# Optimization experiments

Hardware: AMD Instinct MI355X
Metric: run time of the kernel (lower is better)

## Reference

```python
import jax, jax.numpy as jnp
import numpy as np

B, P, F, H, C, D = 512, 32, 16, 4, 32, 128   # graphs, nodes/graph, node feat, heads, head_dim, hidden
N = B * P
E_DIM = 5

def _lin(k, o, i):
    return jax.random.normal(k, (o, i)) * (1.0 / np.sqrt(i))

def setup_inputs():
    key = jax.random.key(0)
    ks = jax.random.split(key, 32)
    # fully-connected directed edges (no self loops) within each graph
    a = np.repeat(np.arange(P), P); b = np.tile(np.arange(P), P)
    m = a != b; a, b = a[m], b[m]
    off = (np.arange(B) * P)[:, None]
    src = (a[None, :] + off).reshape(-1); dst = (b[None, :] + off).reshape(-1)
    edge_index = jnp.asarray(np.stack([src, dst]), dtype=jnp.int32)
    E = src.size
    x = jax.random.normal(ks[0], (N, F))
    edge_attr = jax.random.normal(ks[1], (E, E_DIM))
    z = jnp.zeros
    return dict(
        x=x, edge_index=edge_index, edge_attr=edge_attr,
        W1l=_lin(ks[2], D, F), b1l=z(D), W1r=_lin(ks[3], D, F), b1r=z(D),
        W1e=_lin(ks[4], D, E_DIM), att1=jax.random.normal(ks[5], (1, H, C)) * 0.1, bias1=z(D),
        W2l=_lin(ks[6], D, D), b2l=z(D), W2r=_lin(ks[7], D, D), b2r=z(D),
        W2e=_lin(ks[8], D, E_DIM), att2=jax.random.normal(ks[9], (1, H, C)) * 0.1, bias2=z(D),
        Wc1=_lin(ks[10], D, D), bc1=z(D), Wc2=_lin(ks[11], 1, D), bc2=z(1),
        Ws1=_lin(ks[12], D, D), bs1=z(D), Ws2=_lin(ks[13], 1, D), bs2=z(1),
        Wn1=_lin(ks[14], D, D), bn1=z(D), Wn2=_lin(ks[15], 1, D), bn2=z(1),
    )

def _gatv2(x, src, dst, edge_attr, Wl, bl, Wr, br, We, att, bias):
    # PyG GATv2Conv, concat=True, heads=H, out_channels=C, edge_dim=E_DIM, add_self_loops=False
    E = src.shape[0]
    xl = x @ Wl.T + bl                                   # [N, H*C] messages (source side)
    xr = x @ Wr.T + br                                   # [N, H*C] destination side
    e = (xl[src] + xr[dst] + edge_attr @ We.T).reshape(E, H, C)
    g = jax.nn.leaky_relu(e, 0.2)
    score = jnp.sum(g * att, axis=-1)                    # [E, H]
    smax = jax.ops.segment_max(score, dst, num_segments=N)
    ex = jnp.exp(score - smax[dst])
    denom = jax.ops.segment_sum(ex, dst, num_segments=N)
    alpha = ex / (denom[dst] + 1e-16)                    # segment softmax over in-edges of dst
    msg = xl[src].reshape(E, H, C) * alpha[..., None]
    return jax.ops.segment_sum(msg, dst, num_segments=N).reshape(N, H * C) + bias

def _mlp(h, W1, b1, W2, b2):
    return jax.nn.relu(h @ W1.T + b1) @ W2.T + b2

def reference(x, edge_index, edge_attr, W1l, b1l, W1r, b1r, W1e, att1, bias1,
              W2l, b2l, W2r, b2r, W2e, att2, bias2,
              Wc1, bc1, Wc2, bc2, Ws1, bs1, Ws2, bs2, Wn1, bn1, Wn2, bn2):
    src, dst = edge_index[0], edge_index[1]
    h = _gatv2(x, src, dst, edge_attr, W1l, b1l, W1r, b1r, W1e, att1, bias1)
    hb = h.reshape(B, P, D)
    h = (hb - hb.mean(axis=1, keepdims=True)).reshape(N, D)   # MeanSubtractionNorm per graph
    h = jax.nn.relu(h)
    h = jax.nn.relu(_gatv2(h, src, dst, edge_attr, W2l, b2l, W2r, b2r, W2e, att2, bias2))
    g = h.reshape(B, P, D).mean(axis=1)                       # global_mean_pool (equal-size graphs)
    value = _mlp(g, Wc1, bc1, Wc2, bc2)                       # critic        [B, 1]
    src_logits = _mlp(h, Ws1, bs1, Ws2, bs2).reshape(B, P)    # source_actor, dense per graph
    noop = _mlp(g, Wn1, bn1, Wn2, bn2)                        # noop_actor    [B, 1]
    return jnp.concatenate([value, noop, src_logits], axis=1) # [B, P+2]
```

## Files before the change

kernel.cpp:

```cpp
#include <hip/hip_runtime.h>

#define PP    32
#define FF    16
#define HH    4
#define CC    32
#define DD    128
#define EDIM  5
#define EPG   992
#define NB    512

template <int CTRL>
__device__ __forceinline__ float dpp_add(float v) {
    int t = __builtin_amdgcn_update_dpp(0, __builtin_bit_cast(int, v), CTRL, 0xF, 0xF, true);
    return v + __builtin_bit_cast(float, t);
}
template <int CTRL>
__device__ __forceinline__ float dpp_mov(float v) {
    int t = __builtin_amdgcn_update_dpp(0, __builtin_bit_cast(int, v), CTRL, 0xF, 0xF, true);
    return __builtin_bit_cast(float, t);
}
__device__ __forceinline__ float red64(float v) {
    v = dpp_add<0x111>(v);
    v = dpp_add<0x112>(v);
    v = dpp_add<0x114>(v);
    v = dpp_add<0x118>(v);
    v = dpp_add<0x142>(v);
    v = dpp_add<0x143>(v);
    return v;
}
__device__ __forceinline__ float redquad(float v) {
    v = dpp_add<0xB1>(v);
    v = dpp_add<0x4E>(v);
    return v;
}
__device__ __forceinline__ float maxquad(float v) {
    v = fmaxf(v, dpp_mov<0xB1>(v));
    v = fmaxf(v, dpp_mov<0x4E>(v));
    return v;
}

__device__ __forceinline__ void attention(const float* __restrict__ eattr,
                                          const float* __restrict__ We, const float* __restrict__ att,
                                          const float* __restrict__ bias,
                                          const float* __restrict__ sMsg, const float* __restrict__ sDst,
                                          float* __restrict__ sS, float* __restrict__ sOut,
                                          int tid, long eBase, bool relu)
{
    float* __restrict__ sE = sOut;
    {
        const int s  = tid >> 4;
        const int ch0 = (tid & 15) * 8;
        float we[40], at[8], xl[8];
#pragma unroll
        for (int q = 0; q < 10; ++q)
            *(float4*)(we + q * 4) = *(const float4*)(We + ch0 * EDIM + q * 4);
        *(float4*)(at)     = *(const float4*)(att + ch0);
        *(float4*)(at + 4) = *(const float4*)(att + ch0 + 4);
        *(float4*)(xl)     = *(const float4*)(sMsg + s * DD + ch0);
        *(float4*)(xl + 4) = *(const float4*)(sMsg + s * DD + ch0 + 4);

        for (int halfd = 0; halfd < 2; ++halfd) {
            const int d0 = halfd * 16;
            {
                const int dl = tid & 15;
                const int d = d0 + dl;
                int jj = d - (d > s);
                if (jj > 30) jj = 30;
                const float* ea = eattr + (eBase + s * 31 + jj) * EDIM;
                const float e0 = ea[0], e1 = ea[1], e2 = ea[2], e3 = ea[3], e4 = ea[4];
                float* p = sE + (((s << 4) | dl) << 3);
                *(float4*)p = make_float4(e0, e1, e2, e3);
                p[4] = e4;
            }
            __syncthreads();
#pragma unroll 2
            for (int dl = 0; dl < 16; ++dl) {
                const int d = d0 + dl;
                const float* ep = sE + (((s << 4) | dl) << 3);
                const float4 ef = *(const float4*)ep;
                const float e4v = ep[4];
                float xr[8];
                *(float4*)(xr)     = *(const float4*)(sDst + d * DD + ch0);
                *(float4*)(xr + 4) = *(const float4*)(sDst + d * DD + ch0 + 4);
                float acc0 = 0.f, acc1 = 0.f;
#pragma unroll
                for (int c = 0; c < 8; ++c) {
                    float v = xl[c] + xr[c];
                    const float* w = we + c * EDIM;
                    v = fmaf(w[0], ef.x, v); v = fmaf(w[1], ef.y, v); v = fmaf(w[2], ef.z, v);
                    v = fmaf(w[3], ef.w, v); v = fmaf(w[4], e4v, v);
                    v = fmaf(0.4f, fabsf(v), 0.6f * v);
                    if (c & 1) acc1 = fmaf(v, at[c], acc1);
                    else       acc0 = fmaf(v, at[c], acc0);
                }
                const float r = redquad(acc0 + acc1);
                if ((tid & 3) == 0)
                    sS[s * DD + d * HH + ((tid >> 2) & 3)] = r;
            }
            __syncthreads();
        }
    }
    {
        const int col = tid >> 2;
        const int r   = tid & 3;
        const int dd  = col >> 2;
        float v[8];
        float mx = -3.4e38f;
#pragma unroll
        for (int i = 0; i < 8; ++i) {
            const int s = r * 8 + i;
            v[i] = sS[s * DD + col];
            mx = (s == dd) ? mx : fmaxf(mx, v[i]);
        }
        mx = maxquad(mx);
        float sum = 0.f;
#pragma unroll
        for (int i = 0; i < 8; ++i) {
            const int s = r * 8 + i;
            float ex = __expf(v[i] - mx);
            ex = (s == dd) ? 0.f : ex;
            v[i] = ex; sum += ex;
        }
        sum = redquad(sum);
        const float inv = 1.f / (sum + 1e-16f);
#pragma unroll
        for (int i = 0; i < 8; ++i)
            sS[(r * 8 + i) * DD + col] = v[i] * inv;
    }
    __syncthreads();
    {
        const int d = tid >> 4, sub = tid & 15;
#pragma unroll
        for (int half = 0; half < 2; ++half) {
            const int ch4 = half * 16 + sub;
            const int idx = d * HH + (ch4 >> 3);
            const float* bp = bias + ch4 * 4;
            float4 acc = make_float4(bp[0], bp[1], bp[2], bp[3]);
#pragma unroll
            for (int s = 0; s < PP; ++s) {
                const float a = sS[s * DD + idx];
                const float4 xv = *(const float4*)(sMsg + s * DD + ch4 * 4);
                acc.x = fmaf(a, xv.x, acc.x);
                acc.y = fmaf(a, xv.y, acc.y);
                acc.z = fmaf(a, xv.z, acc.z);
                acc.w = fmaf(a, xv.w, acc.w);
            }
            if (relu) {
                acc.x = fmaxf(acc.x, 0.f); acc.y = fmaxf(acc.y, 0.f);
                acc.z = fmaxf(acc.z, 0.f); acc.w = fmaxf(acc.w, 0.f);
            }
            *(float4*)(sOut + d * DD + ch4 * 4) = acc;
        }
    }
}

extern "C" __global__ void __launch_bounds__(512)
__attribute__((amdgpu_waves_per_eu(4, 4)))
planetwars_gnn_kernel(const float* __restrict__ x, const float* __restrict__ eattr,
                      const float* __restrict__ W1l, const float* __restrict__ b1l,
                      const float* __restrict__ W1r, const float* __restrict__ b1r,
                      const float* __restrict__ W1e, const float* __restrict__ att1, const float* __restrict__ bias1,
                      const float* __restrict__ W2l, const float* __restrict__ b2l,
                      const float* __restrict__ W2r, const float* __restrict__ b2r,
                      const float* __restrict__ W2e, const float* __restrict__ att2, const float* __restrict__ bias2,
                      const float* __restrict__ Wc1, const float* __restrict__ bc1,
                      const float* __restrict__ Wc2, const float* __restrict__ bc2,
                      const float* __restrict__ Ws1, const float* __restrict__ bs1,
                      const float* __restrict__ Ws2, const float* __restrict__ bs2,
                      const float* __restrict__ Wn1, const float* __restrict__ bn1,
                      const float* __restrict__ Wn2, const float* __restrict__ bn2,
                      float* __restrict__ out)
{
    __shared__ __align__(16) float sA[PP * DD];
    __shared__ __align__(16) float sB[PP * DD];
    __shared__ __align__(16) float sH[PP * DD];
    __shared__ __align__(16) float sU[PP * DD];

    const int tid = threadIdx.x;
    const int g = blockIdx.x;
    const long eBase = (long)g * EPG;

    sU[tid] = x[g * PP * FF + tid];
    __syncthreads();

    {
        const int j = tid & 127, d0 = (tid >> 7) * 8;
        float wl[16], wr[16];
#pragma unroll
        for (int q = 0; q < 4; ++q) {
            *(float4*)(wl + q * 4) = *(const float4*)(W1l + j * FF + q * 4);
            *(float4*)(wr + q * 4) = *(const float4*)(W1r + j * FF + q * 4);
        }
        const float bl = b1l[j], br = b1r[j];
#pragma unroll
        for (int i = 0; i < 8; ++i) {
            const float* xr = sU + (d0 + i) * FF;
            float al = bl, ar = br;
#pragma unroll
            for (int k = 0; k < FF; ++k) {
                const float xv = xr[k];
                al = fmaf(wl[k], xv, al);
                ar = fmaf(wr[k], xv, ar);
            }
            sA[(d0 + i) * DD + j] = al;
            sB[(d0 + i) * DD + j] = ar;
        }
    }
    __syncthreads();

    attention(eattr, W1e, att1, bias1, sA, sB, sU, sH, tid, eBase, false);
    __syncthreads();

    {
        const int col = tid >> 2, r = tid & 3;
        float v[8];
        float ssum = 0.f;
#pragma unroll
        for (int i = 0; i < 8; ++i) {
            v[i] = sH[(r * 8 + i) * DD + col];
            ssum += v[i];
        }
        ssum = redquad(ssum);
        const float mn = ssum * (1.0f / 32.0f);
#pragma unroll
        for (int i = 0; i < 8; ++i)
            sH[(r * 8 + i) * DD + col] = fmaxf(v[i] - mn, 0.f);
    }
    __syncthreads();

    {
        const int jj = tid & 63, d0 = (tid >> 6) * 4;
        float accL0[4], accL1[4], accR0[4], accR1[4];
        const float bl0 = b2l[jj], bl1 = b2l[jj + 64];
        const float br0 = b2r[jj], br1 = b2r[jj + 64];
#pragma unroll
        for (int i = 0; i < 4; ++i) { accL0[i] = bl0; accL1[i] = bl1; accR0[i] = br0; accR1[i] = br1; }
        const float* WL0 = W2l + jj * DD;
        const float* WL1 = W2l + (jj + 64) * DD;
        const float* WR0 = W2r + jj * DD;
        const float* WR1 = W2r + (jj + 64) * DD;
        for (int k8 = 0; k8 < 16; ++k8) {
            const float4 l00 = *(const float4*)(WL0 + k8 * 8), l01 = *(const float4*)(WL0 + k8 * 8 + 4);
            const float4 l10 = *(const float4*)(WL1 + k8 * 8), l11 = *(const float4*)(WL1 + k8 * 8 + 4);
            const float4 r00 = *(const float4*)(WR0 + k8 * 8), r01 = *(const float4*)(WR0 + k8 * 8 + 4);
            const float4 r10 = *(const float4*)(WR1 + k8 * 8), r11 = *(const float4*)(WR1 + k8 * 8 + 4);
#pragma unroll
            for (int i = 0; i < 4; ++i) {
                const float4 a0 = *(const float4*)(sH + (d0 + i) * DD + k8 * 8);
                const float4 a1 = *(const float4*)(sH + (d0 + i) * DD + k8 * 8 + 4);
                accL0[i] = fmaf(l00.x, a0.x, accL0[i]); accL0[i] = fmaf(l00.y, a0.y, accL0[i]);
                accL0[i] = fmaf(l00.z, a0.z, accL0[i]); accL0[i] = fmaf(l00.w, a0.w, accL0[i]);
                accL0[i] = fmaf(l01.x, a1.x, accL0[i]); accL0[i] = fmaf(l01.y, a1.y, accL0[i]);
                accL0[i] = fmaf(l01.z, a1.z, accL0[i]); accL0[i] = fmaf(l01.w, a1.w, accL0[i]);
                accL1[i] = fmaf(l10.x, a0.x, accL1[i]); accL1[i] = fmaf(l10.y, a0.y, accL1[i]);
                accL1[i] = fmaf(l10.z, a0.z, accL1[i]); accL1[i] = fmaf(l10.w, a0.w, accL1[i]);
                accL1[i] = fmaf(l11.x, a1.x, accL1[i]); accL1[i] = fmaf(l11.y, a1.y, accL1[i]);
                accL1[i] = fmaf(l11.z, a1.z, accL1[i]); accL1[i] = fmaf(l11.w, a1.w, accL1[i]);
                accR0[i] = fmaf(r00.x, a0.x, accR0[i]); accR0[i] = fmaf(r00.y, a0.y, accR0[i]);
                accR0[i] = fmaf(r00.z, a0.z, accR0[i]); accR0[i] = fmaf(r00.w, a0.w, accR0[i]);
                accR0[i] = fmaf(r01.x, a1.x, accR0[i]); accR0[i] = fmaf(r01.y, a1.y, accR0[i]);
                accR0[i] = fmaf(r01.z, a1.z, accR0[i]); accR0[i] = fmaf(r01.w, a1.w, accR0[i]);
                accR1[i] = fmaf(r10.x, a0.x, accR1[i]); accR1[i] = fmaf(r10.y, a0.y, accR1[i]);
                accR1[i] = fmaf(r10.z, a0.z, accR1[i]); accR1[i] = fmaf(r10.w, a0.w, accR1[i]);
                accR1[i] = fmaf(r11.x, a1.x, accR1[i]); accR1[i] = fmaf(r11.y, a1.y, accR1[i]);
                accR1[i] = fmaf(r11.z, a1.z, accR1[i]); accR1[i] = fmaf(r11.w, a1.w, accR1[i]);
            }
        }
#pragma unroll
        for (int i = 0; i < 4; ++i) {
            sA[(d0 + i) * DD + jj]      = accL0[i];
            sA[(d0 + i) * DD + jj + 64] = accL1[i];
            sB[(d0 + i) * DD + jj]      = accR0[i];
            sB[(d0 + i) * DD + jj + 64] = accR1[i];
        }
    }
    __syncthreads();

    attention(eattr, W2e, att2, bias2, sA, sB, sU, sH, tid, eBase, true);
    __syncthreads();

    {
        const int col = tid >> 2, r = tid & 3;
        float ssum = 0.f;
#pragma unroll
        for (int i = 0; i < 8; ++i) ssum += sH[(r * 8 + i) * DD + col];
        ssum = redquad(ssum);
        if (r == 0) sU[col] = ssum * (1.0f / 32.0f);
    }
    __syncthreads();

    {
        const int jj = tid & 63, d0 = (tid >> 6) * 4;
        const float b0 = bs1[jj], b1 = bs1[jj + 64];
        float acc0[4], acc1[4];
#pragma unroll
        for (int i = 0; i < 4; ++i) { acc0[i] = b0; acc1[i] = b1; }
        const float* W0 = Ws1 + jj * DD;
        const float* W1 = Ws1 + (jj + 64) * DD;
        for (int k8 = 0; k8 < 16; ++k8) {
            const float4 w00 = *(const float4*)(W0 + k8 * 8), w01 = *(const float4*)(W0 + k8 * 8 + 4);
            const float4 w10 = *(const float4*)(W1 + k8 * 8), w11 = *(const float4*)(W1 + k8 * 8 + 4);
#pragma unroll
            for (int i = 0; i < 4; ++i) {
                const float4 a0 = *(const float4*)(sH + (d0 + i) * DD + k8 * 8);
                const float4 a1 = *(const float4*)(sH + (d0 + i) * DD + k8 * 8 + 4);
                acc0[i] = fmaf(w00.x, a0.x, acc0[i]); acc0[i] = fmaf(w00.y, a0.y, acc0[i]);
                acc0[i] = fmaf(w00.z, a0.z, acc0[i]); acc0[i] = fmaf(w00.w, a0.w, acc0[i]);
                acc0[i] = fmaf(w01.x, a1.x, acc0[i]); acc0[i] = fmaf(w01.y, a1.y, acc0[i]);
                acc0[i] = fmaf(w01.z, a1.z, acc0[i]); acc0[i] = fmaf(w01.w, a1.w, acc0[i]);
                acc1[i] = fmaf(w10.x, a0.x, acc1[i]); acc1[i] = fmaf(w10.y, a0.y, acc1[i]);
                acc1[i] = fmaf(w10.z, a0.z, acc1[i]); acc1[i] = fmaf(w10.w, a0.w, acc1[i]);
                acc1[i] = fmaf(w11.x, a1.x, acc1[i]); acc1[i] = fmaf(w11.y, a1.y, acc1[i]);
                acc1[i] = fmaf(w11.z, a1.z, acc1[i]); acc1[i] = fmaf(w11.w, a1.w, acc1[i]);
            }
        }
        const float ws2a = Ws2[jj], ws2b = Ws2[jj + 64];
        const float bias2s = bs2[0];
#pragma unroll
        for (int i = 0; i < 4; ++i) {
            const float t = fmaf(fmaxf(acc0[i], 0.f), ws2a, fmaxf(acc1[i], 0.f) * ws2b);
            const float r = red64(t);
            if ((tid & 63) == 63) out[g * 34 + 2 + d0 + i] = r + bias2s;
        }
    }

    if (tid < 128) {
        const int w = tid >> 6, j = tid & 63;
        const float* Wa = (w ? Wn1 : Wc1);
        const float* ba = (w ? bn1 : bc1);
        const float* Wb = (w ? Wn2 : Wc2);
        const float  bb = (w ? bn2 : bc2)[0];
        float h0 = ba[j], h1 = ba[j + 64];
        const float* R0 = Wa + j * DD;
        const float* R1 = Wa + (j + 64) * DD;
#pragma unroll
        for (int k8 = 0; k8 < 16; ++k8) {
            const float4 g0 = *(const float4*)(sU + k8 * 8);
            const float4 g1 = *(const float4*)(sU + k8 * 8 + 4);
            const float4 p00 = *(const float4*)(R0 + k8 * 8), p01 = *(const float4*)(R0 + k8 * 8 + 4);
            const float4 p10 = *(const float4*)(R1 + k8 * 8), p11 = *(const float4*)(R1 + k8 * 8 + 4);
            h0 = fmaf(p00.x, g0.x, h0); h0 = fmaf(p00.y, g0.y, h0);
            h0 = fmaf(p00.z, g0.z, h0); h0 = fmaf(p00.w, g0.w, h0);
            h0 = fmaf(p01.x, g1.x, h0); h0 = fmaf(p01.y, g1.y, h0);
            h0 = fmaf(p01.z, g1.z, h0); h0 = fmaf(p01.w, g1.w, h0);
            h1 = fmaf(p10.x, g0.x, h1); h1 = fmaf(p10.y, g0.y, h1);
            h1 = fmaf(p10.z, g0.z, h1); h1 = fmaf(p10.w, g0.w, h1);
            h1 = fmaf(p11.x, g1.x, h1); h1 = fmaf(p11.y, g1.y, h1);
            h1 = fmaf(p11.z, g1.z, h1); h1 = fmaf(p11.w, g1.w, h1);
        }
        const float t = fmaf(fmaxf(h0, 0.f), Wb[j], fmaxf(h1, 0.f) * Wb[j + 64]);
        const float r = red64(t);
        if (j == 63) out[g * 34 + w] = r + bb;
    }
}

extern "C" void kernel_launch(void* const* d_in, const int* in_sizes, int n_in,
                              void* d_out, int out_size, void* d_ws, size_t ws_size,
                              hipStream_t stream)
{
    (void)in_sizes; (void)n_in; (void)d_ws; (void)ws_size; (void)out_size;
    planetwars_gnn_kernel<<<dim3(NB), dim3(512), 0, stream>>>(
        (const float*)d_in[0], (const float*)d_in[2],
        (const float*)d_in[3], (const float*)d_in[4], (const float*)d_in[5], (const float*)d_in[6],
        (const float*)d_in[7], (const float*)d_in[8], (const float*)d_in[9],
        (const float*)d_in[10], (const float*)d_in[11], (const float*)d_in[12], (const float*)d_in[13],
        (const float*)d_in[14], (const float*)d_in[15], (const float*)d_in[16],
        (const float*)d_in[17], (const float*)d_in[18], (const float*)d_in[19], (const float*)d_in[20],
        (const float*)d_in[21], (const float*)d_in[22], (const float*)d_in[23], (const float*)d_in[24],
        (const float*)d_in[25], (const float*)d_in[26], (const float*)d_in[27], (const float*)d_in[28],
        (float*)d_out);
}
```

Baseline: 244.7 us.

## Split fused GNN kernel into multi-kernel pipeline via workspace buffers

Replaces the single per-graph fused kernel with ten smaller launches (transforms, score, softmax, aggregation, norm, heads) that exchange intermediates through global workspace buffers. The score stage is split across two blocks per graph to raise parallelism and relieve per-block LDS/register pressure. The monolithic kernel is kept as a fallback when no workspace is provided. This adds global memory round trips and several launch overheads in exchange for more blocks and simpler kernels.

```diff
diff --git a/kernel.cpp b/kernel.cpp
--- a/kernel.cpp
+++ b/kernel.cpp
@@ -8,6 +8,9 @@
 #define EDIM  5
 #define EPG   992
 #define NB    512
+#define NN    (NB * PP)
+#define WS_SLOT 2097152
+#define WS_NEED ((size_t)4 * WS_SLOT * 4)
 
 template <int CTRL>
 __device__ __forceinline__ float dpp_add(float v) {
@@ -20,12 +23,8 @@
     return __builtin_bit_cast(float, t);
 }
 __device__ __forceinline__ float red64(float v) {
-    v = dpp_add<0x111>(v);
-    v = dpp_add<0x112>(v);
-    v = dpp_add<0x114>(v);
-    v = dpp_add<0x118>(v);
-    v = dpp_add<0x142>(v);
-    v = dpp_add<0x143>(v);
+    v = dpp_add<0x111>(v); v = dpp_add<0x112>(v); v = dpp_add<0x114>(v);
+    v = dpp_add<0x118>(v); v = dpp_add<0x142>(v); v = dpp_add<0x143>(v);
     return v;
 }
 __device__ __forceinline__ float redquad(float v) {
@@ -39,7 +38,306 @@
     return v;
 }
 
-__device__ __forceinline__ void attention(const float* __restrict__ eattr,
+
+extern "C" __global__ void __launch_bounds__(256)
+k_t1(const float* __restrict__ x,
+     const float* __restrict__ W1l, const float* __restrict__ b1l,
+     const float* __restrict__ W1r, const float* __restrict__ b1r,
+     float* __restrict__ xl, float* __restrict__ xr)
+{
+    const int idx = blockIdx.x * 256 + threadIdx.x;
+    const int n = idx >> 7, j = idx & 127;
+    float wl[16], wr[16], xv[16];
+#pragma unroll
+    for (int q = 0; q < 4; ++q) {
+        *(float4*)(wl + q * 4) = *(const float4*)(W1l + j * FF + q * 4);
+        *(float4*)(wr + q * 4) = *(const float4*)(W1r + j * FF + q * 4);
+        *(float4*)(xv + q * 4) = *(const float4*)(x + n * FF + q * 4);
+    }
+    float al = b1l[j], ar = b1r[j];
+#pragma unroll
+    for (int k = 0; k < FF; ++k) {
+        al = fmaf(wl[k], xv[k], al);
+        ar = fmaf(wr[k], xv[k], ar);
+    }
+    xl[idx] = al;
+    xr[idx] = ar;
+}
+
+extern "C" __global__ void __launch_bounds__(512)
+k_score(const float* __restrict__ xl, const float* __restrict__ xr,
+        const float* __restrict__ eattr,
+        const float* __restrict__ We, const float* __restrict__ att,
+        float* __restrict__ sc)
+{
+    const int b = blockIdx.x;
+    const int g = b >> 1, halfd = b & 1;
+    const int tid = threadIdx.x;
+    const int s   = tid >> 4;
+    const int h   = (tid >> 2) & 3;
+    const int ch0 = (tid & 15) * 8;
+    const long eBase = (long)g * EPG;
+
+    float we[40], at[8], xlv[8];
+#pragma unroll
+    for (int q = 0; q < 10; ++q)
+        *(float4*)(we + q * 4) = *(const float4*)(We + ch0 * EDIM + q * 4);
+    *(float4*)(at)      = *(const float4*)(att + ch0);
+    *(float4*)(at + 4)  = *(const float4*)(att + ch0 + 4);
+    *(float4*)(xlv)     = *(const float4*)(xl + (g * PP + s) * DD + ch0);
+    *(float4*)(xlv + 4) = *(const float4*)(xl + (g * PP + s) * DD + ch0 + 4);
+
+    const int d0 = halfd * 16;
+    for (int dl = 0; dl < 16; ++dl) {
+        const int d = d0 + dl;
+        int jj = d - (d > s);
+        if (jj > 30) jj = 30;
+        const float* ea = eattr + (eBase + s * 31 + jj) * EDIM;
+        const float e0 = ea[0], e1 = ea[1], e2 = ea[2], e3 = ea[3], e4 = ea[4];
+        float xrv[8];
+        *(float4*)(xrv)     = *(const float4*)(xr + (g * PP + d) * DD + ch0);
+        *(float4*)(xrv + 4) = *(const float4*)(xr + (g * PP + d) * DD + ch0 + 4);
+        float acc0 = 0.f, acc1 = 0.f;
+#pragma unroll
+        for (int c = 0; c < 8; ++c) {
+            float v = xlv[c] + xrv[c];
+            const float* w = we + c * EDIM;
+            v = fmaf(w[0], e0, v); v = fmaf(w[1], e1, v); v = fmaf(w[2], e2, v);
+            v = fmaf(w[3], e3, v); v = fmaf(w[4], e4, v);
+            v = fmaf(0.4f, fabsf(v), 0.6f * v);
+            if (c & 1) acc1 = fmaf(v, at[c], acc1);
+            else       acc0 = fmaf(v, at[c], acc0);
+        }
+        const float r = redquad(acc0 + acc1);
+        if ((tid & 3) == 0)
+            sc[(((long)(g * PP + d) << 2) + h) * PP + s] = r;
+    }
+}
+
+extern "C" __global__ void __launch_bounds__(256)
+k_softmax(float* __restrict__ sc)
+{
+    const int idx = blockIdx.x * 256 + threadIdx.x;
+    const int col = idx >> 2;
+    const int r   = idx & 3;
+    const int dd  = (col >> 2) & 31;
+    float* base = sc + (long)col * PP;
+    float v[8];
+    float mx = -3.4e38f;
+#pragma unroll
+    for (int i = 0; i < 8; ++i) {
+        const int s = r * 8 + i;
+        v[i] = base[s];
+        mx = (s == dd) ? mx : fmaxf(mx, v[i]);
+    }
+    mx = maxquad(mx);
+    float sum = 0.f;
+#pragma unroll
+    for (int i = 0; i < 8; ++i) {
+        const int s = r * 8 + i;
+        float ex = __expf(v[i] - mx);
+        ex = (s == dd) ? 0.f : ex;
+        v[i] = ex; sum += ex;
+    }
+    sum = redquad(sum);
+    const float inv = 1.f / (sum + 1e-16f);
+#pragma unroll
+    for (int i = 0; i < 8; ++i)
+        base[r * 8 + i] = v[i] * inv;
+}
+
+extern "C" __global__ void __launch_bounds__(256)
+k_agg(const float* __restrict__ alpha, const float* __restrict__ msg,
+      const float* __restrict__ bias, float* __restrict__ hout, const int relu)
+{
+    const int idx = blockIdx.x * 256 + threadIdx.x;
+    const int n = idx >> 5, ch4 = idx & 31;
+    const int g = n >> 5;
+    const int h = ch4 >> 3;
+    const float* ap = alpha + (((long)n << 2) + h) * PP;
+    const float* bp = bias + ch4 * 4;
+    float4 acc = make_float4(bp[0], bp[1], bp[2], bp[3]);
+#pragma unroll
+    for (int s = 0; s < PP; ++s) {
+        const float a = ap[s];
+        const float4 xv = *(const float4*)(msg + (g * PP + s) * DD + ch4 * 4);
+        acc.x = fmaf(a, xv.x, acc.x);
+        acc.y = fmaf(a, xv.y, acc.y);
+        acc.z = fmaf(a, xv.z, acc.z);
+        acc.w = fmaf(a, xv.w, acc.w);
+    }
+    if (relu) {
+        acc.x = fmaxf(acc.x, 0.f); acc.y = fmaxf(acc.y, 0.f);
+        acc.z = fmaxf(acc.z, 0.f); acc.w = fmaxf(acc.w, 0.f);
+    }
+    *(float4*)(hout + (long)n * DD + ch4 * 4) = acc;
+}
+
+extern "C" __global__ void __launch_bounds__(256)
+k_norm(float* __restrict__ h)
+{
+    const int idx = blockIdx.x * 256 + threadIdx.x;
+    const int colg = idx >> 2;
+    const int r = idx & 3;
+    const int g = colg >> 7, col = colg & 127;
+    float v[8];
+    float ssum = 0.f;
+#pragma unroll
+    for (int i = 0; i < 8; ++i) {
+        v[i] = h[(long)(g * PP + r * 8 + i) * DD + col];
+        ssum += v[i];
+    }
+    ssum = redquad(ssum);
+    const float mn = ssum * (1.0f / 32.0f);
+#pragma unroll
+    for (int i = 0; i < 8; ++i)
+        h[(long)(g * PP + r * 8 + i) * DD + col] = fmaxf(v[i] - mn, 0.f);
+}
+
+extern "C" __global__ void __launch_bounds__(512)
+k_t2(const float* __restrict__ h,
+     const float* __restrict__ W2l, const float* __restrict__ b2l,
+     const float* __restrict__ W2r, const float* __restrict__ b2r,
+     float* __restrict__ xl, float* __restrict__ xr)
+{
+    const int g = blockIdx.x, tid = threadIdx.x;
+    const int jj = tid & 63, d0 = (tid >> 6) * 4;
+    const float* hb = h + (long)g * PP * DD;
+    float accL0[4], accL1[4], accR0[4], accR1[4];
+    const float bl0 = b2l[jj], bl1 = b2l[jj + 64];
+    const float br0 = b2r[jj], br1 = b2r[jj + 64];
+#pragma unroll
+    for (int i = 0; i < 4; ++i) { accL0[i] = bl0; accL1[i] = bl1; accR0[i] = br0; accR1[i] = br1; }
+    const float* WL0 = W2l + jj * DD;
+    const float* WL1 = W2l + (jj + 64) * DD;
+    const float* WR0 = W2r + jj * DD;
+    const float* WR1 = W2r + (jj + 64) * DD;
+    for (int k8 = 0; k8 < 16; ++k8) {
+        const float4 l00 = *(const float4*)(WL0 + k8 * 8), l01 = *(const float4*)(WL0 + k8 * 8 + 4);
+        const float4 l10 = *(const float4*)(WL1 + k8 * 8), l11 = *(const float4*)(WL1 + k8 * 8 + 4);
+        const float4 r00 = *(const float4*)(WR0 + k8 * 8), r01 = *(const float4*)(WR0 + k8 * 8 + 4);
+        const float4 r10 = *(const float4*)(WR1 + k8 * 8), r11 = *(const float4*)(WR1 + k8 * 8 + 4);
+#pragma unroll
+        for (int i = 0; i < 4; ++i) {
+            const float4 a0 = *(const float4*)(hb + (d0 + i) * DD + k8 * 8);
+            const float4 a1 = *(const float4*)(hb + (d0 + i) * DD + k8 * 8 + 4);
+            accL0[i] = fmaf(l00.x, a0.x, accL0[i]); accL0[i] = fmaf(l00.y, a0.y, accL0[i]);
+            accL0[i] = fmaf(l00.z, a0.z, accL0[i]); accL0[i] = fmaf(l00.w, a0.w, accL0[i]);
+            accL0[i] = fmaf(l01.x, a1.x, accL0[i]); accL0[i] = fmaf(l01.y, a1.y, accL0[i]);
+            accL0[i] = fmaf(l01.z, a1.z, accL0[i]); accL0[i] = fmaf(l01.w, a1.w, accL0[i]);
+            accL1[i] = fmaf(l10.x, a0.x, accL1[i]); accL1[i] = fmaf(l10.y, a0.y, accL1[i]);
+            accL1[i] = fmaf(l10.z, a0.z, accL1[i]); accL1[i] = fmaf(l10.w, a0.w, accL1[i]);
+            accL1[i] = fmaf(l11.x, a1.x, accL1[i]); accL1[i] = fmaf(l11.y, a1.y, accL1[i]);
+            accL1[i] = fmaf(l11.z, a1.z, accL1[i]); accL1[i] = fmaf(l11.w, a1.w, accL1[i]);
+            accR0[i] = fmaf(r00.x, a0.x, accR0[i]); accR0[i] = fmaf(r00.y, a0.y, accR0[i]);
+            accR0[i] = fmaf(r00.z, a0.z, accR0[i]); accR0[i] = fmaf(r00.w, a0.w, accR0[i]);
+            accR0[i] = fmaf(r01.x, a1.x, accR0[i]); accR0[i] = fmaf(r01.y, a1.y, accR0[i]);
+            accR0[i] = fmaf(r01.z, a1.z, accR0[i]); accR0[i] = fmaf(r01.w, a1.w, accR0[i]);
+            accR1[i] = fmaf(r10.x, a0.x, accR1[i]); accR1[i] = fmaf(r10.y, a0.y, accR1[i]);
+            accR1[i] = fmaf(r10.z, a0.z, accR1[i]); accR1[i] = fmaf(r10.w, a0.w, accR1[i]);
+            accR1[i] = fmaf(r11.x, a1.x, accR1[i]); accR1[i] = fmaf(r11.y, a1.y, accR1[i]);
+            accR1[i] = fmaf(r11.z, a1.z, accR1[i]); accR1[i] = fmaf(r11.w, a1.w, accR1[i]);
+        }
+    }
+#pragma unroll
+    for (int i = 0; i < 4; ++i) {
+        xl[(long)(g * PP + d0 + i) * DD + jj]      = accL0[i];
+        xl[(long)(g * PP + d0 + i) * DD + jj + 64] = accL1[i];
+        xr[(long)(g * PP + d0 + i) * DD + jj]      = accR0[i];
+        xr[(long)(g * PP + d0 + i) * DD + jj + 64] = accR1[i];
+    }
+}
+
+extern "C" __global__ void __launch_bounds__(512)
+k_heads(const float* __restrict__ h2,
+        const float* __restrict__ Wc1, const float* __restrict__ bc1,
+        const float* __restrict__ Wc2, const float* __restrict__ bc2,
+        const float* __restrict__ Ws1, const float* __restrict__ bs1,
+        const float* __restrict__ Ws2, const float* __restrict__ bs2,
+        const float* __restrict__ Wn1, const float* __restrict__ bn1,
+        const float* __restrict__ Wn2, const float* __restrict__ bn2,
+        float* __restrict__ out)
+{
+    __shared__ __align__(16) float sU[DD];
+    const int g = blockIdx.x, tid = threadIdx.x;
+    const float* hb = h2 + (long)g * PP * DD;
+
+    {
+        const int col = tid >> 2, r = tid & 3;
+        float ssum = 0.f;
+#pragma unroll
+        for (int i = 0; i < 8; ++i) ssum += hb[(r * 8 + i) * DD + col];
+        ssum = redquad(ssum);
+        if (r == 0) sU[col] = ssum * (1.0f / 32.0f);
+    }
+    __syncthreads();
+
+    {
+        const int jj = tid & 63, d0 = (tid >> 6) * 4;
+        const float b0 = bs1[jj], b1 = bs1[jj + 64];
+        float acc0[4], acc1[4];
+#pragma unroll
+        for (int i = 0; i < 4; ++i) { acc0[i] = b0; acc1[i] = b1; }
+        const float* W0 = Ws1 + jj * DD;
+        const float* W1 = Ws1 + (jj + 64) * DD;
+        for (int k8 = 0; k8 < 16; ++k8) {
+            const float4 w00 = *(const float4*)(W0 + k8 * 8), w01 = *(const float4*)(W0 + k8 * 8 + 4);
+            const float4 w10 = *(const float4*)(W1 + k8 * 8), w11 = *(const float4*)(W1 + k8 * 8 + 4);
+#pragma unroll
+            for (int i = 0; i < 4; ++i) {
+                const float4 a0 = *(const float4*)(hb + (d0 + i) * DD + k8 * 8);
+                const float4 a1 = *(const float4*)(hb + (d0 + i) * DD + k8 * 8 + 4);
+                acc0[i] = fmaf(w00.x, a0.x, acc0[i]); acc0[i] = fmaf(w00.y, a0.y, acc0[i]);
+                acc0[i] = fmaf(w00.z, a0.z, acc0[i]); acc0[i] = fmaf(w00.w, a0.w, acc0[i]);
+                acc0[i] = fmaf(w01.x, a1.x, acc0[i]); acc0[i] = fmaf(w01.y, a1.y, acc0[i]);
+                acc0[i] = fmaf(w01.z, a1.z, acc0[i]); acc0[i] = fmaf(w01.w, a1.w, acc0[i]);
+                acc1[i] = fmaf(w10.x, a0.x, acc1[i]); acc1[i] = fmaf(w10.y, a0.y, acc1[i]);
+                acc1[i] = fmaf(w10.z, a0.z, acc1[i]); acc1[i] = fmaf(w10.w, a0.w, acc1[i]);
+                acc1[i] = fmaf(w11.x, a1.x, acc1[i]); acc1[i] = fmaf(w11.y, a1.y, acc1[i]);
+                acc1[i] = fmaf(w11.z, a1.z, acc1[i]); acc1[i] = fmaf(w11.w, a1.w, acc1[i]);
+            }
+        }
+        const float ws2a = Ws2[jj], ws2b = Ws2[jj + 64];
+        const float bias2s = bs2[0];
+#pragma unroll
+        for (int i = 0; i < 4; ++i) {
+            const float t = fmaf(fmaxf(acc0[i], 0.f), ws2a, fmaxf(acc1[i], 0.f) * ws2b);
+            const float r = red64(t);
+            if ((tid & 63) == 63) out[g * 34 + 2 + d0 + i] = r + bias2s;
+        }
+    }
+
+    if (tid < 128) {
+        const int w = tid >> 6, j = tid & 63;
+        const float* Wa = (w ? Wn1 : Wc1);
+        const float* ba = (w ? bn1 : bc1);
+        const float* Wb = (w ? Wn2 : Wc2);
+        const float  bb = (w ? bn2 : bc2)[0];
+        float h0 = ba[j], h1 = ba[j + 64];
+        const float* R0 = Wa + j * DD;
+        const float* R1 = Wa + (j + 64) * DD;
+#pragma unroll
+        for (int k8 = 0; k8 < 16; ++k8) {
+            const float4 g0 = *(const float4*)(sU + k8 * 8);
+            const float4 g1 = *(const float4*)(sU + k8 * 8 + 4);
+            const float4 p00 = *(const float4*)(R0 + k8 * 8), p01 = *(const float4*)(R0 + k8 * 8 + 4);
+            const float4 p10 = *(const float4*)(R1 + k8 * 8), p11 = *(const float4*)(R1 + k8 * 8 + 4);
+            h0 = fmaf(p00.x, g0.x, h0); h0 = fmaf(p00.y, g0.y, h0);
+            h0 = fmaf(p00.z, g0.z, h0); h0 = fmaf(p00.w, g0.w, h0);
+            h0 = fmaf(p01.x, g1.x, h0); h0 = fmaf(p01.y, g1.y, h0);
+            h0 = fmaf(p01.z, g1.z, h0); h0 = fmaf(p01.w, g1.w, h0);
+            h1 = fmaf(p10.x, g0.x, h1); h1 = fmaf(p10.y, g0.y, h1);
+            h1 = fmaf(p10.z, g0.z, h1); h1 = fmaf(p10.w, g0.w, h1);
+            h1 = fmaf(p11.x, g1.x, h1); h1 = fmaf(p11.y, g1.y, h1);
+            h1 = fmaf(p11.z, g1.z, h1); h1 = fmaf(p11.w, g1.w, h1);
+        }
+        const float t = fmaf(fmaxf(h0, 0.f), Wb[j], fmaxf(h1, 0.f) * Wb[j + 64]);
+        const float r = red64(t);
+        if (j == 63) out[g * 34 + w] = r + bb;
+    }
+}
+
+__device__ __forceinline__ void mono_attention(const float* __restrict__ eattr,
                                           const float* __restrict__ We, const float* __restrict__ att,
                                           const float* __restrict__ bias,
                                           const float* __restrict__ sMsg, const float* __restrict__ sDst,
@@ -58,7 +356,6 @@
         *(float4*)(at + 4) = *(const float4*)(att + ch0 + 4);
         *(float4*)(xl)     = *(const float4*)(sMsg + s * DD + ch0);
         *(float4*)(xl + 4) = *(const float4*)(sMsg + s * DD + ch0 + 4);
-
         for (int halfd = 0; halfd < 2; ++halfd) {
             const int d0 = halfd * 16;
             {
@@ -73,7 +370,6 @@
                 p[4] = e4;
             }
             __syncthreads();
-#pragma unroll 2
             for (int dl = 0; dl < 16; ++dl) {
                 const int d = d0 + dl;
                 const float* ep = sE + (((s << 4) | dl) << 3);
@@ -155,34 +451,30 @@
 }
 
 extern "C" __global__ void __launch_bounds__(512)
-__attribute__((amdgpu_waves_per_eu(4, 4)))
-planetwars_gnn_kernel(const float* __restrict__ x, const float* __restrict__ eattr,
-                      const float* __restrict__ W1l, const float* __restrict__ b1l,
-                      const float* __restrict__ W1r, const float* __restrict__ b1r,
-                      const float* __restrict__ W1e, const float* __restrict__ att1, const float* __restrict__ bias1,
-                      const float* __restrict__ W2l, const float* __restrict__ b2l,
-                      const float* __restrict__ W2r, const float* __restrict__ b2r,
-                      const float* __restrict__ W2e, const float* __restrict__ att2, const float* __restrict__ bias2,
-                      const float* __restrict__ Wc1, const float* __restrict__ bc1,
-                      const float* __restrict__ Wc2, const float* __restrict__ bc2,
-                      const float* __restrict__ Ws1, const float* __restrict__ bs1,
-                      const float* __restrict__ Ws2, const float* __restrict__ bs2,
-                      const float* __restrict__ Wn1, const float* __restrict__ bn1,
-                      const float* __restrict__ Wn2, const float* __restrict__ bn2,
-                      float* __restrict__ out)
+planetwars_gnn_mono(const float* __restrict__ x, const float* __restrict__ eattr,
+                    const float* __restrict__ W1l, const float* __restrict__ b1l,
+                    const float* __restrict__ W1r, const float* __restrict__ b1r,
+                    const float* __restrict__ W1e, const float* __restrict__ att1, const float* __restrict__ bias1,
+                    const float* __restrict__ W2l, const float* __restrict__ b2l,
+                    const float* __restrict__ W2r, const float* __restrict__ b2r,
+                    const float* __restrict__ W2e, const float* __restrict__ att2, const float* __restrict__ bias2,
+                    const float* __restrict__ Wc1, const float* __restrict__ bc1,
+                    const float* __restrict__ Wc2, const float* __restrict__ bc2,
+                    const float* __restrict__ Ws1, const float* __restrict__ bs1,
+                    const float* __restrict__ Ws2, const float* __restrict__ bs2,
+                    const float* __restrict__ Wn1, const float* __restrict__ bn1,
+                    const float* __restrict__ Wn2, const float* __restrict__ bn2,
+                    float* __restrict__ out)
 {
     __shared__ __align__(16) float sA[PP * DD];
     __shared__ __align__(16) float sB[PP * DD];
     __shared__ __align__(16) float sH[PP * DD];
     __shared__ __align__(16) float sU[PP * DD];
-
     const int tid = threadIdx.x;
     const int g = blockIdx.x;
     const long eBase = (long)g * EPG;
-
     sU[tid] = x[g * PP * FF + tid];
     __syncthreads();
-
     {
         const int j = tid & 127, d0 = (tid >> 7) * 8;
         float wl[16], wr[16];
@@ -207,10 +499,8 @@
         }
     }
     __syncthreads();
-
-    attention(eattr, W1e, att1, bias1, sA, sB, sU, sH, tid, eBase, false);
-    __syncthreads();
-
+    mono_attention(eattr, W1e, att1, bias1, sA, sB, sU, sH, tid, eBase, false);
+    __syncthreads();
     {
         const int col = tid >> 2, r = tid & 3;
         float v[8];
@@ -227,7 +517,6 @@
             sH[(r * 8 + i) * DD + col] = fmaxf(v[i] - mn, 0.f);
     }
     __syncthreads();
-
     {
         const int jj = tid & 63, d0 = (tid >> 6) * 4;
         float accL0[4], accL1[4], accR0[4], accR1[4];
@@ -275,10 +564,8 @@
         }
     }
     __syncthreads();
-
-    attention(eattr, W2e, att2, bias2, sA, sB, sU, sH, tid, eBase, true);
-    __syncthreads();
-
+    mono_attention(eattr, W2e, att2, bias2, sA, sB, sU, sH, tid, eBase, true);
+    __syncthreads();
     {
         const int col = tid >> 2, r = tid & 3;
         float ssum = 0.f;
@@ -288,7 +575,6 @@
         if (r == 0) sU[col] = ssum * (1.0f / 32.0f);
     }
     __syncthreads();
-
     {
         const int jj = tid & 63, d0 = (tid >> 6) * 4;
         const float b0 = bs1[jj], b1 = bs1[jj + 64];
@@ -323,7 +609,6 @@
             if ((tid & 63) == 63) out[g * 34 + 2 + d0 + i] = r + bias2s;
         }
     }
-
     if (tid < 128) {
         const int w = tid >> 6, j = tid & 63;
         const float* Wa = (w ? Wn1 : Wc1);
@@ -358,15 +643,46 @@
                               void* d_out, int out_size, void* d_ws, size_t ws_size,
                               hipStream_t stream)
 {
-    (void)in_sizes; (void)n_in; (void)d_ws; (void)ws_size; (void)out_size;
-    planetwars_gnn_kernel<<<dim3(NB), dim3(512), 0, stream>>>(
-        (const float*)d_in[0], (const float*)d_in[2],
-        (const float*)d_in[3], (const float*)d_in[4], (const float*)d_in[5], (const float*)d_in[6],
-        (const float*)d_in[7], (const float*)d_in[8], (const float*)d_in[9],
-        (const float*)d_in[10], (const float*)d_in[11], (const float*)d_in[12], (const float*)d_in[13],
-        (const float*)d_in[14], (const float*)d_in[15], (const float*)d_in[16],
-        (const float*)d_in[17], (const float*)d_in[18], (const float*)d_in[19], (const float*)d_in[20],
-        (const float*)d_in[21], (const float*)d_in[22], (const float*)d_in[23], (const float*)d_in[24],
-        (const float*)d_in[25], (const float*)d_in[26], (const float*)d_in[27], (const float*)d_in[28],
-        (float*)d_out);
-}
+    (void)in_sizes; (void)n_in; (void)out_size;
+    const float* x     = (const float*)d_in[0];
+    const float* eattr = (const float*)d_in[2];
+    const float *W1l = (const float*)d_in[3],  *b1l = (const float*)d_in[4];
+    const float *W1r = (const float*)d_in[5],  *b1r = (const float*)d_in[6];
+    const float *W1e = (const float*)d_in[7],  *att1 = (const float*)d_in[8],  *bias1 = (const float*)d_in[9];
+    const float *W2l = (const float*)d_in[10], *b2l = (const float*)d_in[11];
+    const float *W2r = (const float*)d_in[12], *b2r = (const float*)d_in[13];
+    const float *W2e = (const float*)d_in[14], *att2 = (const float*)d_in[15], *bias2 = (const float*)d_in[16];
+    const float *Wc1 = (const float*)d_in[17], *bc1 = (const float*)d_in[18];
+    const float *Wc2 = (const float*)d_in[19], *bc2 = (const float*)d_in[20];
+    const float *Ws1 = (const float*)d_in[21], *bs1 = (const float*)d_in[22];
+    const float *Ws2 = (const float*)d_in[23], *bs2 = (const float*)d_in[24];
+    const float *Wn1 = (const float*)d_in[25], *bn1 = (const float*)d_in[26];
+    const float *Wn2 = (const float*)d_in[27], *bn2 = (const float*)d_in[28];
+    float* out = (float*)d_out;
+
+    if (d_ws == nullptr || ws_size < WS_NEED) {
+        planetwars_gnn_mono<<<dim3(NB), dim3(512), 0, stream>>>(
+            x, eattr, W1l, b1l, W1r, b1r, W1e, att1, bias1,
+            W2l, b2l, W2r, b2r, W2e, att2, bias2,
+            Wc1, bc1, Wc2, bc2, Ws1, bs1, Ws2, bs2, Wn1, bn1, Wn2, bn2, out);
+        return;
+    }
+
+    float* B0 = (float*)d_ws;
+    float* B1 = B0 + WS_SLOT;
+    float* B2 = B0 + 2 * (long)WS_SLOT;
+    float* B3 = B0 + 3 * (long)WS_SLOT;
+
+    k_t1     <<<dim3(NN * DD / 256), dim3(256), 0, stream>>>(x, W1l, b1l, W1r, b1r, B0, B1);
+    k_score  <<<dim3(NB * 2),        dim3(512), 0, stream>>>(B0, B1, eattr, W1e, att1, B2);
+    k_softmax<<<dim3(1024),          dim3(256), 0, stream>>>(B2);
+    k_agg    <<<dim3(2048),          dim3(256), 0, stream>>>(B2, B0, bias1, B3, 0);
+    k_norm   <<<dim3(1024),          dim3(256), 0, stream>>>(B3);
+    k_t2     <<<dim3(NB),            dim3(512), 0, stream>>>(B3, W2l, b2l, W2r, b2r, B0, B1);
+    k_score  <<<dim3(NB * 2),        dim3(512), 0, stream>>>(B0, B1, eattr, W2e, att2, B2);
+    k_softmax<<<dim3(1024),          dim3(256), 0, stream>>>(B2);
+    k_agg    <<<dim3(2048),          dim3(256), 0, stream>>>(B2, B0, bias2, B3, 1);
+    k_heads  <<<dim3(NB),            dim3(512), 0, stream>>>(B3, Wc1, bc1, Wc2, bc2,
+                                                             Ws1, bs1, Ws2, bs2,
+                                                             Wn1, bn1, Wn2, bn2, out);
+}
```

After: 373.0 us. 52.4% more time.
